# Kernel optimization log

Measured on AMD Instinct MI355X. Metric: run time of the kernel, lower is better.

## Reference

```python
import jax, jax.numpy as jnp
import numpy as np


def setup_inputs() -> dict:
    key = jax.random.key(0)
    ks = jax.random.split(key, 8)
    N, D, G, H = 131072, 128, 2048, 512
    features = jax.random.normal(ks[0], (N, D), dtype=jnp.float32)
    graph_index = jnp.sort(jax.random.randint(ks[1], (N,), 0, G))
    s1 = 1.0 / np.sqrt(D)
    W_m = jax.random.uniform(ks[2], (H, D), jnp.float32, -s1, s1)
    b_m = jax.random.uniform(ks[3], (H,), jnp.float32, -s1, s1)
    s2 = 1.0 / np.sqrt(H)
    W_ih = jax.random.uniform(ks[4], (4 * H, 2 * H), jnp.float32, -s2, s2)
    W_hh = jax.random.uniform(ks[5], (4 * H, H), jnp.float32, -s2, s2)
    b_ih = jax.random.uniform(ks[6], (4 * H,), jnp.float32, -s2, s2)
    b_hh = jax.random.uniform(ks[7], (4 * H,), jnp.float32, -s2, s2)
    return dict(features=features, graph_index=graph_index, W_m=W_m, b_m=b_m,
                W_ih=W_ih, W_hh=W_hh, b_ih=b_ih, b_hh=b_hh, num_graphs=G)


def reference(features, graph_index, W_m, b_m, W_ih, W_hh, b_ih, b_hh, num_graphs):
    H = W_m.shape[0]
    LOOP = 3
    EPS = 1e-7
    NEG_BIG = -1e10
    m = features @ W_m.T + b_m                      # [N, H]
    h = jnp.zeros((num_graphs, H), m.dtype)
    c = jnp.zeros((num_graphs, H), m.dtype)
    q_star = jnp.zeros((num_graphs, 2 * H), m.dtype)
    for _ in range(LOOP):
        # PyTorch LSTMCell: gates in (i, f, g, o) order
        gates = q_star @ W_ih.T + h @ W_hh.T + (b_ih + b_hh)   # [G, 4H]
        i_g, f_g, g_g, o_g = jnp.split(gates, 4, axis=-1)
        c = jax.nn.sigmoid(f_g) * c + jax.nn.sigmoid(i_g) * jnp.tanh(g_g)
        h = jax.nn.sigmoid(o_g) * jnp.tanh(c)
        # attention scores per node against its graph's query h
        e = jnp.sum(m * h[graph_index], axis=-1, keepdims=True)  # [N, 1]
        e_max = jax.ops.segment_max(e, graph_index, num_segments=num_graphs)
        e_max = jax.lax.stop_gradient(
            jnp.where(jnp.isfinite(e_max), e_max, NEG_BIG))
        e = e - e_max[graph_index]
        exp_e = jnp.exp(jnp.clip(e, -30.0, 20.0))
        exp_sum = jax.ops.segment_sum(exp_e, graph_index, num_segments=num_graphs)
        a = exp_e / (exp_sum[graph_index] + EPS)                 # [N, 1]
        r = jax.ops.segment_sum(m * a, graph_index, num_segments=num_graphs)  # [G, H]
        q_star = jnp.concatenate([h, r], axis=-1)                # [G, 2H]
    return q_star
```

## Files before the change

kernel.cpp:

```cpp
#include <hip/hip_runtime.h>

#define N_NODES 131072
#define DIM     128
#define NG      2048
#define HD      512

typedef unsigned short u16;
typedef _Float16 half8 __attribute__((ext_vector_type(8)));
typedef float  f32x4  __attribute__((ext_vector_type(4)));

__device__ u16   g_wm[(size_t)HD * DIM];
__device__ u16   g_wmT[(size_t)DIM * HD];
__device__ u16   g_wgf[(size_t)2048 * 640];
__device__ u16   g_wih2[(size_t)2048 * 512];
__device__ float g_bc[2048];
__device__ float g_bf[2048];
__device__ float g_gh[2048];
__device__ float g_c0[512];
__device__ float g_w20[128];
__device__ float g_tp[NG];
__device__ u16   g_Acat[(size_t)NG * 640];
__device__ u16   g_h3[(size_t)NG * HD];
__device__ float g_c[(size_t)NG * HD];
__device__ int   g_start[NG + 1];
__device__ int   g_isbf16;
__device__ int   g_idx64;

__device__ __forceinline__ float bf2f(u16 u) {
  unsigned v = ((unsigned)u) << 16;
  float f; __builtin_memcpy(&f, &v, 4); return f;
}
__device__ __forceinline__ float u2f_hi(unsigned u) {
  unsigned v = u & 0xFFFF0000u;
  float f; __builtin_memcpy(&f, &v, 4); return f;
}
__device__ __forceinline__ float u2f_lo(unsigned u) {
  unsigned v = u << 16;
  float f; __builtin_memcpy(&f, &v, 4); return f;
}
__device__ __forceinline__ u16 f2bf(float f) {
  unsigned u; __builtin_memcpy(&u, &f, 4);
  u += 0x7FFFu + ((u >> 16) & 1u);
  return (u16)(u >> 16);
}
__device__ __forceinline__ u16 f2h(float f) {
  _Float16 h = (_Float16)f; u16 u; __builtin_memcpy(&u, &h, 2); return u;
}
__device__ __forceinline__ float h2f(u16 u) {
  _Float16 h; __builtin_memcpy(&h, &u, 2); return (float)h;
}
__device__ __forceinline__ float rdf(const void* p, int i) {
  return g_isbf16 ? bf2f(((const u16*)p)[i]) : ((const float*)p)[i];
}

#define GLD16(gp, lp) __builtin_amdgcn_global_load_lds(                          \
    (const __attribute__((address_space(1))) void*)(gp),                         \
    (__attribute__((address_space(3))) void*)(lp), 16, 0, 0)

__global__ void k_detect(const void* feat, const void* gi) {
  __shared__ int cnt;
  if (threadIdx.x == 0) cnt = 0;
  __syncthreads();
  u16 u = ((const u16*)feat)[threadIdx.x];
  float v = bf2f(u);
  float a = fabsf(v);
  int ok = (v == v) && a >= 1e-6f && a <= 1e6f;
  atomicAdd(&cnt, ok);
  __syncthreads();
  if (threadIdx.x == 0) {
    g_isbf16 = (cnt >= 230);
    g_idx64 = (((const int*)gi)[N_NODES - 1] == 0);
  }
}

#define NWP ((size_t)HD * DIM / 2)
#define NWT ((size_t)DIM * HD / 2)
#define NW1 ((size_t)2048 * 512 / 2)
#define NW2 ((size_t)2048 * 512 / 2)
#define W_PAIRS (NWP + NWT + NW1 + NW2)

__global__ __launch_bounds__(256) void k_s0(const void* gidxv, const void* wmp,
                                            const void* wih, const void* whh) {
  const int t = threadIdx.x;
  for (size_t i = (size_t)blockIdx.x * 256 + t; i < W_PAIRS;
       i += (size_t)gridDim.x * 256) {
    if (i < NWP) {
      float v0, v1;
      if (g_isbf16) {
        unsigned pr = ((const unsigned*)wmp)[i];
        v0 = bf2f((u16)pr); v1 = bf2f((u16)(pr >> 16));
      } else {
        float2 v = ((const float2*)wmp)[i];
        v0 = v.x; v1 = v.y;
      }
      ((unsigned*)g_wm)[i] = (unsigned)f2h(v0) | ((unsigned)f2h(v1) << 16);
    } else if (i < NWP + NWT) {
      size_t p = i - NWP;
      int d = (int)(p >> 8), j = (int)(p & 255) * 2;
      float v0 = rdf(wmp, j * DIM + d);
      float v1 = rdf(wmp, (j + 1) * DIM + d);
      ((unsigned*)g_wmT)[(size_t)d * 256 + (j >> 1)] =
          (unsigned)f2h(v0) | ((unsigned)f2h(v1) << 16);
    } else if (i < NWP + NWT + NW1) {
      size_t p = i - NWP - NWT;
      int n = (int)(p >> 8), kp = (int)(p & 255), k = kp * 2;
      int orig = (n & 3) * 512 + (n >> 2);
      float v0 = rdf(wih, orig * 1024 + k)     + rdf(whh, orig * 512 + k);
      float v1 = rdf(wih, orig * 1024 + k + 1) + rdf(whh, orig * 512 + k + 1);
      ((unsigned*)g_wgf)[(size_t)n * 320 + kp] =
          (unsigned)f2h(v0) | ((unsigned)f2h(v1) << 16);
    } else {
      size_t p = i - NWP - NWT - NW1;
      int n = (int)(p >> 8), kp = (int)(p & 255), k = kp * 2;
      int orig = (n & 3) * 512 + (n >> 2);
      float v0 = rdf(wih, orig * 1024 + 512 + k);
      float v1 = rdf(wih, orig * 1024 + 512 + k + 1);
      ((unsigned*)g_wih2)[(size_t)n * 256 + kp] =
          (unsigned)f2h(v0) | ((unsigned)f2h(v1) << 16);
    }
  }
  if (blockIdx.x < 512) {
    int n = blockIdx.x * 256 + t;
    const int idx64 = g_idx64;
    int gg = idx64 ? (int)((const long long*)gidxv)[n] : ((const int*)gidxv)[n];
    if (n == 0) {
      for (int x = 0; x <= gg; ++x) g_start[x] = 0;
    } else {
      int gp = idx64 ? (int)((const long long*)gidxv)[n - 1] : ((const int*)gidxv)[n - 1];
      for (int x = gp + 1; x <= gg; ++x) g_start[x] = n;
    }
    if (n == N_NODES - 1) {
      for (int x = gg + 1; x <= NG; ++x) g_start[x] = N_NODES;
    }
  }
}

__global__ __launch_bounds__(256) void k_s1(const void* bih, const void* bhh,
                                            const void* bm) {
  alignas(16) __shared__ char smem[16384];
  const int t = threadIdx.x, b = blockIdx.x;
  if (b < 128) {
    float* s_bm = (float*)smem;
    float* s_h0 = s_bm + 512;
    for (int p = t; p < 512; p += 256) {
      s_bm[p] = rdf(bm, p);
      float xi = rdf(bih, p)        + rdf(bhh, p);
      float xg = rdf(bih, p + 1024) + rdf(bhh, p + 1024);
      float xo = rdf(bih, p + 1536) + rdf(bhh, p + 1536);
      float si = 1.f / (1.f + __expf(-xi));
      float tg = tanhf(xg);
      float so = 1.f / (1.f + __expf(-xo));
      s_h0[p] = so * tanhf(si * tg);
    }
    __syncthreads();
    const int rloc = t >> 4, k = t & 15;
    const int n = b * 16 + rloc;
    float sbf = 0.f, sgh = 0.f;
#pragma unroll
    for (int j = 0; j < 4; ++j) {
      const int e = k * 8 + j * 128;
      half8 w2v = *(const half8*)(g_wih2 + (size_t)n * 512 + e);
      half8 w1v = *(const half8*)(g_wgf  + (size_t)n * 640 + e);
#pragma unroll
      for (int d = 0; d < 8; ++d) {
        sbf += (float)w2v[d] * s_bm[e + d];
        sgh += (float)w1v[d] * s_h0[e + d];
      }
    }
#pragma unroll
    for (int o = 1; o < 16; o <<= 1) {
      sbf += __shfl_xor(sbf, o, 64);
      sgh += __shfl_xor(sgh, o, 64);
    }
    if (k == 0) {
      const int orig = (n & 3) * 512 + (n >> 2);
      g_bf[n] = sbf;
      g_gh[n] = sgh;
      g_bc[n] = rdf(bih, orig) + rdf(bhh, orig);
    }
  } else if (b < 192) {
    u16* As = (u16*)smem;
    u16* Bs = As + 4096;
    const int bx = b - 128;
    const int lid = t & 63, w = t >> 6;
    const int m0 = (bx & 31) * 64, n0 = (bx >> 5) * 64;
    const int rr = lid & 15, quad = lid >> 4;
    const int rsub = lid >> 3;
    const int cs = (lid & 7) ^ rsub;
    const int wm = (w >> 1) * 32, wn = (w & 1) * 32;
    f32x4 acc[2][2] = {};
    for (int kt = 0; kt < 8; ++kt) {
      const int k0 = kt * 64;
      GLD16(g_wih2 + (size_t)(m0 + w * 16 + rsub) * 512 + k0 + cs * 8, As + (w * 16) * 64);
      GLD16(g_wih2 + (size_t)(m0 + w * 16 + 8 + rsub) * 512 + k0 + cs * 8, As + (w * 16 + 8) * 64);
      GLD16(g_wmT + (size_t)(n0 + w * 16 + rsub) * 512 + k0 + cs * 8, Bs + (w * 16) * 64);
      GLD16(g_wmT + (size_t)(n0 + w * 16 + 8 + rsub) * 512 + k0 + cs * 8, Bs + (w * 16 + 8) * 64);
      __syncthreads();
#pragma unroll
      for (int kk = 0; kk < 2; ++kk) {
        const int qb = kk * 4 + quad;
        const int sw = (qb ^ (rr & 7)) << 3;
        half8 af[2], bfr[2];
#pragma unroll
        for (int i = 0; i < 2; ++i) af[i]  = *(const half8*)(As + (wm + i * 16 + rr) * 64 + sw);
#pragma unroll
        for (int j = 0; j < 2; ++j) bfr[j] = *(const half8*)(Bs + (wn + j * 16 + rr) * 64 + sw);
#pragma unroll
        for (int i = 0; i < 2; ++i)
#pragma unroll
          for (int j = 0; j < 2; ++j)
            acc[i][j] = __builtin_amdgcn_mfma_f32_16x16x32_f16(bfr[j], af[i], acc[i][j], 0, 0, 0);
      }
      __syncthreads();
    }
#pragma unroll
    for (int i = 0; i < 2; ++i)
#pragma unroll
      for (int j = 0; j < 2; ++j) {
        const int row = m0 + wm + i * 16 + rr;
        const int c0 = n0 + wn + j * 16 + quad * 4;
        u16 h4[4];
#pragma unroll
        for (int r = 0; r < 4; ++r) h4[r] = f2h(acc[i][j][r]);
        *(uint2*)(g_wgf + (size_t)row * 640 + 512 + c0) =
            make_uint2((unsigned)h4[0] | ((unsigned)h4[1] << 16),
                       (unsigned)h4[2] | ((unsigned)h4[3] << 16));
      }
  } else if (b == 192) {
    float* s_h   = (float*)smem;
    float* s_red = s_h + 512;
    for (int j = t; j < 512; j += 256) {
      float xi = rdf(bih, j)        + rdf(bhh, j);
      float xg = rdf(bih, j + 1024) + rdf(bhh, j + 1024);
      float xo = rdf(bih, j + 1536) + rdf(bhh, j + 1536);
      float si = 1.f / (1.f + __expf(-xi));
      float tg = tanhf(xg);
      float so = 1.f / (1.f + __expf(-xo));
      float cn = si * tg;
      float hn = so * tanhf(cn);
      g_c0[j] = cn;
      s_h[j] = hn;
    }
    __syncthreads();
    const int dg = t & 15, jg = t >> 4;
    float a8[8] = {};
    for (int jj = 0; jj < 32; ++jj) {
      const int j = jg * 32 + jj;
      half8 wv = *(const half8*)(g_wm + (size_t)j * 128 + dg * 8);
      const float hv = s_h[j];
#pragma unroll
      for (int d = 0; d < 8; ++d) a8[d] += hv * (float)wv[d];
    }
#pragma unroll
    for (int d = 0; d < 8; ++d) {
      a8[d] += __shfl_xor(a8[d], 16, 64);
      a8[d] += __shfl_xor(a8[d], 32, 64);
    }
    const int w = t >> 6;
    if ((t & 63) < 16) {
      *(f32x4*)&s_red[w * 128 + dg * 8]     = *(f32x4*)&a8[0];
      *(f32x4*)&s_red[w * 128 + dg * 8 + 4] = *(f32x4*)&a8[4];
    }
    __syncthreads();
    if (t < 128)
      g_w20[t] = s_red[t] + s_red[128 + t] + s_red[256 + t] + s_red[384 + t];
  }
}

__global__ __launch_bounds__(256) void k_gemm(int ktiles2, int aoff, int useGh,
                                              int first, int wout, int h3out,
                                              void* __restrict__ out) {
  alignas(16) __shared__ u16 As[2][64 * 64];
  alignas(16) __shared__ u16 Bs[2][64 * 64];
  const int t = threadIdx.x, lid = t & 63, w = t >> 6;
  const int m0 = (blockIdx.x & 31) * 64, n0 = (blockIdx.x >> 5) * 64;
  const int rr = lid & 15, quad = lid >> 4;
  const int rsub = lid >> 3;
  const int cs = (lid & 7) ^ rsub;
  const int wm = (w >> 1) * 32, wn = (w & 1) * 32;
  const int isb = g_isbf16;
  f32x4 acc[2][2] = {};
  for (int kt2 = 0; kt2 < ktiles2; ++kt2) {
#pragma unroll
    for (int b = 0; b < 2; ++b) {
      const int k0 = aoff + (kt2 * 2 + b) * 64;
      GLD16(g_Acat + (size_t)(m0 + w * 16 + rsub) * 640 + k0 + cs * 8, As[b] + (w * 16) * 64);
      GLD16(g_Acat + (size_t)(m0 + w * 16 + 8 + rsub) * 640 + k0 + cs * 8, As[b] + (w * 16 + 8) * 64);
      GLD16(g_wgf  + (size_t)(n0 + w * 16 + rsub) * 640 + k0 + cs * 8, Bs[b] + (w * 16) * 64);
      GLD16(g_wgf  + (size_t)(n0 + w * 16 + 8 + rsub) * 640 + k0 + cs * 8, Bs[b] + (w * 16 + 8) * 64);
    }
    __syncthreads();
#pragma unroll
    for (int b = 0; b < 2; ++b)
#pragma unroll
      for (int kk = 0; kk < 2; ++kk) {
        const int qb = kk * 4 + quad;
        const int sw = (qb ^ (rr & 7)) << 3;
        half8 af[2], bfr[2];
#pragma unroll
        for (int i = 0; i < 2; ++i) af[i]  = *(const half8*)(As[b] + (wm + i * 16 + rr) * 64 + sw);
#pragma unroll
        for (int j = 0; j < 2; ++j) bfr[j] = *(const half8*)(Bs[b] + (wn + j * 16 + rr) * 64 + sw);
#pragma unroll
        for (int i = 0; i < 2; ++i)
#pragma unroll
          for (int j = 0; j < 2; ++j)
            acc[i][j] = __builtin_amdgcn_mfma_f32_16x16x32_f16(bfr[j], af[i], acc[i][j], 0, 0, 0);
      }
    __syncthreads();
  }
#pragma unroll
  for (int i = 0; i < 2; ++i) {
    const int row = m0 + wm + i * 16 + rr;
    const float tp = g_tp[row];
#pragma unroll
    for (int j = 0; j < 2; ++j) {
      const int c0 = n0 + wn + j * 16 + quad * 4;
      const int jj = c0 >> 2;
      float4 bc = *(const float4*)(g_bc + c0);
      float4 bf = *(const float4*)(g_bf + c0);
      float gx = 0.f, gy = 0.f, gz = 0.f, gw = 0.f;
      if (useGh) {
        float4 gh = *(const float4*)(g_gh + c0);
        gx = gh.x; gy = gh.y; gz = gh.z; gw = gh.w;
      }
      float xi = acc[i][j][0] + bc.x + gx + tp * bf.x;
      float xf = acc[i][j][1] + bc.y + gy + tp * bf.y;
      float xg = acc[i][j][2] + bc.z + gz + tp * bf.z;
      float xo = acc[i][j][3] + bc.w + gw + tp * bf.w;
      float si = 1.f / (1.f + __expf(-xi));
      float sf = 1.f / (1.f + __expf(-xf));
      float tg = tanhf(xg);
      float so = 1.f / (1.f + __expf(-xo));
      float cp = first ? g_c0[jj] : g_c[(size_t)row * 512 + jj];
      float cn = sf * cp + si * tg;
      float hn = so * tanhf(cn);
      g_c[(size_t)row * 512 + jj] = cn;
      if (h3out) g_h3[(size_t)row * 512 + jj] = f2h(hn);
      else       g_Acat[(size_t)row * 640 + jj] = f2h(hn);
      if (wout) {
        if (isb) ((u16*)out)[(size_t)row * 1024 + jj] = f2bf(hn);
        else     ((float*)out)[(size_t)row * 1024 + jj] = hn;
      }
    }
  }
}

__global__ __launch_bounds__(256) void k_attn(const void* __restrict__ feat, int mode,
                                              int hsel, int fin,
                                              void* __restrict__ out,
                                              const void* __restrict__ bm) {
  __shared__ float s_m[4], s_l[4];
  __shared__ float s_s[4][DIM];
  __shared__ float s_h[512];
  __shared__ float s_keep[DIM];
  __shared__ float s_tpv[1];
  const int g = blockIdx.x;
  const int t = threadIdx.x, lid = t & 63, wid = t >> 6;
  const int c = lid & 15;
  const int slot = lid >> 4;
  const int israw = g_isbf16;
  const int s = g_start[g], e = g_start[g + 1];
  float w2r[8];
  if (mode) {
    const u16* hsrc = hsel ? g_h3 : g_Acat;
    const int hstr = hsel ? 512 : 640;
    for (int p = t; p < 512; p += 256)
      s_h[p] = h2f(hsrc[(size_t)g * hstr + p]);
    __syncthreads();
    const int jg = t >> 4;
    float a8[8] = {};
    for (int jj = 0; jj < 32; ++jj) {
      const int j = jg * 32 + jj;
      half8 wv = *(const half8*)(g_wm + (size_t)j * 128 + c * 8);
      const float hv = s_h[j];
#pragma unroll
      for (int d = 0; d < 8; ++d) a8[d] += hv * (float)wv[d];
    }
#pragma unroll
    for (int d = 0; d < 8; ++d) {
      a8[d] += __shfl_xor(a8[d], 16, 64);
      a8[d] += __shfl_xor(a8[d], 32, 64);
    }
    if (lid < 16) {
      *(f32x4*)&s_s[wid][c * 8]     = *(f32x4*)&a8[0];
      *(f32x4*)&s_s[wid][c * 8 + 4] = *(f32x4*)&a8[4];
    }
    __syncthreads();
#pragma unroll
    for (int d = 0; d < 8; ++d)
      w2r[d] = s_s[0][c * 8 + d] + s_s[1][c * 8 + d] +
               s_s[2][c * 8 + d] + s_s[3][c * 8 + d];
    __syncthreads();
  } else {
    *(float4*)(w2r)     = *(const float4*)(g_w20 + c * 8);
    *(float4*)(w2r + 4) = *(const float4*)(g_w20 + c * 8 + 4);
  }
  float mrun = -3.0e38f, lsum = 0.f;
  float racc[8] = {0.f, 0.f, 0.f, 0.f, 0.f, 0.f, 0.f, 0.f};
  for (int nb = s + wid * 4; nb < e; nb += 16) {
    const int n = nb + slot;
    float fv[8], d;
    if (n < e) {
      if (israw) {
        uint4 q = *(const uint4*)((const u16*)feat + (size_t)n * DIM + c * 8);
        fv[0] = u2f_lo(q.x); fv[1] = u2f_hi(q.x);
        fv[2] = u2f_lo(q.y); fv[3] = u2f_hi(q.y);
        fv[4] = u2f_lo(q.z); fv[5] = u2f_hi(q.z);
        fv[6] = u2f_lo(q.w); fv[7] = u2f_hi(q.w);
      } else {
        const float* fp = (const float*)feat + (size_t)n * DIM + c * 8;
        float4 f0 = *(const float4*)fp;
        float4 f1 = *(const float4*)(fp + 4);
        fv[0] = f0.x; fv[1] = f0.y; fv[2] = f0.z; fv[3] = f0.w;
        fv[4] = f1.x; fv[5] = f1.y; fv[6] = f1.z; fv[7] = f1.w;
      }
      d = 0.f;
#pragma unroll
      for (int j = 0; j < 8; ++j) d += fv[j] * w2r[j];
    } else {
      d = -1.0e30f;
#pragma unroll
      for (int j = 0; j < 8; ++j) fv[j] = 0.f;
    }
#pragma unroll
    for (int o = 1; o < 16; o <<= 1) d += __shfl_xor(d, o, 64);
    float m4 = fmaxf(d, __shfl_xor(d, 16, 64));
    m4 = fmaxf(m4, __shfl_xor(m4, 32, 64));
    float mnew = fmaxf(mrun, m4);
    float sc = __expf(mrun - mnew);
    float w = __expf(d - mnew);
    lsum = lsum * sc + w;
#pragma unroll
    for (int j = 0; j < 8; ++j) racc[j] = racc[j] * sc + w * fv[j];
    mrun = mnew;
  }
  float lt = lsum + __shfl_xor(lsum, 16, 64);
  lt += __shfl_xor(lt, 32, 64);
#pragma unroll
  for (int j = 0; j < 8; ++j) {
    racc[j] += __shfl_xor(racc[j], 16, 64);
    racc[j] += __shfl_xor(racc[j], 32, 64);
  }
  if (lid == 0) s_m[wid] = mrun;
  __syncthreads();
  float gmax = fmaxf(fmaxf(s_m[0], s_m[1]), fmaxf(s_m[2], s_m[3]));
  float scw = __expf(mrun - gmax);
  if (lid < 16) {
    float4 lo = make_float4(racc[0] * scw, racc[1] * scw, racc[2] * scw, racc[3] * scw);
    float4 hi = make_float4(racc[4] * scw, racc[5] * scw, racc[6] * scw, racc[7] * scw);
    *(f32x4*)&s_s[wid][c * 8] = *(f32x4*)&lo;
    *(f32x4*)&s_s[wid][c * 8 + 4] = *(f32x4*)&hi;
  }
  if (lid == 0) s_l[wid] = lt * scw;
  __syncthreads();
  float total = s_l[0] + s_l[1] + s_l[2] + s_l[3];
  float inv = 1.f / (total + 1e-7f);
  if (!fin) {
    if (t == 0) g_tp[g] = total * inv;
    if (t < 64) {
      int d0 = t * 2;
      float v0 = (s_s[0][d0] + s_s[1][d0] + s_s[2][d0] + s_s[3][d0]) * inv;
      float v1 = (s_s[0][d0 + 1] + s_s[1][d0 + 1] + s_s[2][d0 + 1] + s_s[3][d0 + 1]) * inv;
      ((unsigned*)g_Acat)[(size_t)g * 320 + 256 + t] =
          (unsigned)f2h(v0) | ((unsigned)f2h(v1) << 16);
    }
  } else {
    if (t == 0) s_tpv[0] = total * inv;
    if (t < 64) {
      int d0 = t * 2;
      s_keep[d0]     = (s_s[0][d0] + s_s[1][d0] + s_s[2][d0] + s_s[3][d0]) * inv;
      s_keep[d0 + 1] = (s_s[0][d0 + 1] + s_s[1][d0 + 1] + s_s[2][d0 + 1] + s_s[3][d0 + 1]) * inv;
    }
    __syncthreads();
    const int jj = t * 2;
    const unsigned* wt = (const unsigned*)g_wmT;
    float a0 = 0.f, a1 = 0.f;
#pragma unroll 8
    for (int d = 0; d < 128; ++d) {
      unsigned pr = wt[d * 256 + t];
      float kv = s_keep[d];
      a0 += kv * h2f((u16)pr);
      a1 += kv * h2f((u16)(pr >> 16));
    }
    float tp = s_tpv[0];
    float r0 = a0 + tp * rdf(bm, jj);
    float r1 = a1 + tp * rdf(bm, jj + 1);
    if (israw) {
      ((unsigned*)out)[((size_t)g * 1024 + 512 + jj) >> 1] =
          (unsigned)f2bf(r0) | ((unsigned)f2bf(r1) << 16);
    } else {
      *(float2*)((float*)out + (size_t)g * 1024 + 512 + jj) = make_float2(r0, r1);
    }
  }
}

extern "C" void kernel_launch(void* const* d_in, const int* in_sizes, int n_in,
                              void* d_out, int out_size, void* d_ws, size_t ws_size,
                              hipStream_t stream) {
  const void* features = d_in[0];
  const void* gidx     = d_in[1];
  const void* W_m      = d_in[2];
  const void* b_m      = d_in[3];
  const void* W_ih     = d_in[4];
  const void* W_hh     = d_in[5];
  const void* b_ih     = d_in[6];
  const void* b_hh     = d_in[7];

  k_detect<<<1, 256, 0, stream>>>(features, gidx);
  k_s0<<<1024, 256, 0, stream>>>(gidx, W_m, W_ih, W_hh);
  k_s1<<<193, 256, 0, stream>>>(b_ih, b_hh, b_m);
  k_attn<<<NG, 256, 0, stream>>>(features, 0, 0, 0, d_out, b_m);
  k_gemm<<<1024, 256, 0, stream>>>(1, 512, 1, 1, 0, 0, d_out);
  k_attn<<<NG, 256, 0, stream>>>(features, 1, 0, 0, d_out, b_m);
  k_gemm<<<1024, 256, 0, stream>>>(5, 0, 0, 0, 1, 1, d_out);
  k_attn<<<NG, 256, 0, stream>>>(features, 1, 1, 1, d_out, b_m);
}
```

Baseline: 224.3 us.

## Batch per-graph h·W_m projection into MFMA GEMM kernel and fold detect into setup

The per-graph projection of h through W_m was computed inside each attention block with scalar FMAs over a 512x128 weight, reading the whole weight once per graph. A separate small MFMA GEMM kernel now computes all [G,128] projections at once into a global buffer, and the attention kernel just loads its row. The dtype/index detection kernel is merged into the first setup kernel, so every block recomputes the flags locally and one launch is removed. This adds two small kernel launches and a global intermediate buffer in exchange for removing the redundant per-block GEMV work.

```diff
diff --git a/kernel.cpp b/kernel.cpp
--- a/kernel.cpp
+++ b/kernel.cpp
@@ -18,6 +18,7 @@
 __device__ float g_gh[2048];
 __device__ float g_c0[512];
 __device__ float g_w20[128];
+__device__ float g_w2[(size_t)NG * DIM];
 __device__ float g_tp[NG];
 __device__ u16   g_Acat[(size_t)NG * 640];
 __device__ u16   g_h3[(size_t)NG * HD];
@@ -52,26 +53,13 @@
 __device__ __forceinline__ float rdf(const void* p, int i) {
   return g_isbf16 ? bf2f(((const u16*)p)[i]) : ((const float*)p)[i];
 }
+__device__ __forceinline__ float rdl(const void* p, int i, int isb) {
+  return isb ? bf2f(((const u16*)p)[i]) : ((const float*)p)[i];
+}
 
 #define GLD16(gp, lp) __builtin_amdgcn_global_load_lds(                          \
     (const __attribute__((address_space(1))) void*)(gp),                         \
     (__attribute__((address_space(3))) void*)(lp), 16, 0, 0)
-
-__global__ void k_detect(const void* feat, const void* gi) {
-  __shared__ int cnt;
-  if (threadIdx.x == 0) cnt = 0;
-  __syncthreads();
-  u16 u = ((const u16*)feat)[threadIdx.x];
-  float v = bf2f(u);
-  float a = fabsf(v);
-  int ok = (v == v) && a >= 1e-6f && a <= 1e6f;
-  atomicAdd(&cnt, ok);
-  __syncthreads();
-  if (threadIdx.x == 0) {
-    g_isbf16 = (cnt >= 230);
-    g_idx64 = (((const int*)gi)[N_NODES - 1] == 0);
-  }
-}
 
 #define NWP ((size_t)HD * DIM / 2)
 #define NWT ((size_t)DIM * HD / 2)
@@ -79,14 +67,30 @@
 #define NW2 ((size_t)2048 * 512 / 2)
 #define W_PAIRS (NWP + NWT + NW1 + NW2)
 
-__global__ __launch_bounds__(256) void k_s0(const void* gidxv, const void* wmp,
-                                            const void* wih, const void* whh) {
+__global__ __launch_bounds__(256) void k_s0(const void* feat, const void* gidxv,
+                                            const void* wmp, const void* wih,
+                                            const void* whh) {
+  __shared__ int s_cnt;
   const int t = threadIdx.x;
+  if (t == 0) s_cnt = 0;
+  __syncthreads();
+  {
+    u16 u = ((const u16*)feat)[t];
+    float v = bf2f(u);
+    float a = fabsf(v);
+    int ok = (v == v) && a >= 1e-6f && a <= 1e6f;
+    atomicAdd(&s_cnt, ok);
+  }
+  __syncthreads();
+  const int isb = (s_cnt >= 230);
+  const int idx64 = (((const int*)gidxv)[N_NODES - 1] == 0);
+  if (blockIdx.x == 0 && t == 0) { g_isbf16 = isb; g_idx64 = idx64; }
+
   for (size_t i = (size_t)blockIdx.x * 256 + t; i < W_PAIRS;
        i += (size_t)gridDim.x * 256) {
     if (i < NWP) {
       float v0, v1;
-      if (g_isbf16) {
+      if (isb) {
         unsigned pr = ((const unsigned*)wmp)[i];
         v0 = bf2f((u16)pr); v1 = bf2f((u16)(pr >> 16));
       } else {
@@ -97,31 +101,30 @@
     } else if (i < NWP + NWT) {
       size_t p = i - NWP;
       int d = (int)(p >> 8), j = (int)(p & 255) * 2;
-      float v0 = rdf(wmp, j * DIM + d);
-      float v1 = rdf(wmp, (j + 1) * DIM + d);
+      float v0 = rdl(wmp, j * DIM + d, isb);
+      float v1 = rdl(wmp, (j + 1) * DIM + d, isb);
       ((unsigned*)g_wmT)[(size_t)d * 256 + (j >> 1)] =
           (unsigned)f2h(v0) | ((unsigned)f2h(v1) << 16);
     } else if (i < NWP + NWT + NW1) {
       size_t p = i - NWP - NWT;
       int n = (int)(p >> 8), kp = (int)(p & 255), k = kp * 2;
       int orig = (n & 3) * 512 + (n >> 2);
-      float v0 = rdf(wih, orig * 1024 + k)     + rdf(whh, orig * 512 + k);
-      float v1 = rdf(wih, orig * 1024 + k + 1) + rdf(whh, orig * 512 + k + 1);
+      float v0 = rdl(wih, orig * 1024 + k, isb)     + rdl(whh, orig * 512 + k, isb);
+      float v1 = rdl(wih, orig * 1024 + k + 1, isb) + rdl(whh, orig * 512 + k + 1, isb);
       ((unsigned*)g_wgf)[(size_t)n * 320 + kp] =
           (unsigned)f2h(v0) | ((unsigned)f2h(v1) << 16);
     } else {
       size_t p = i - NWP - NWT - NW1;
       int n = (int)(p >> 8), kp = (int)(p & 255), k = kp * 2;
       int orig = (n & 3) * 512 + (n >> 2);
-      float v0 = rdf(wih, orig * 1024 + 512 + k);
-      float v1 = rdf(wih, orig * 1024 + 512 + k + 1);
+      float v0 = rdl(wih, orig * 1024 + 512 + k, isb);
+      float v1 = rdl(wih, orig * 1024 + 512 + k + 1, isb);
       ((unsigned*)g_wih2)[(size_t)n * 256 + kp] =
           (unsigned)f2h(v0) | ((unsigned)f2h(v1) << 16);
     }
   }
   if (blockIdx.x < 512) {
     int n = blockIdx.x * 256 + t;
-    const int idx64 = g_idx64;
     int gg = idx64 ? (int)((const long long*)gidxv)[n] : ((const int*)gidxv)[n];
     if (n == 0) {
       for (int x = 0; x <= gg; ++x) g_start[x] = 0;
@@ -267,6 +270,52 @@
   }
 }
 
+__global__ __launch_bounds__(256) void k_w2(int hsel) {
+  alignas(16) __shared__ u16 As[64 * 64];
+  alignas(16) __shared__ u16 Bs[64 * 64];
+  const int t = threadIdx.x, lid = t & 63, w = t >> 6;
+  const int m0 = blockIdx.x * 64, n0 = blockIdx.y * 64;
+  const int rr = lid & 15, quad = lid >> 4;
+  const int rsub = lid >> 3;
+  const int cs = (lid & 7) ^ rsub;
+  const int wm = (w >> 1) * 32, wn = (w & 1) * 32;
+  const u16* Ap = hsel ? g_h3 : g_Acat;
+  const int astr = hsel ? 512 : 640;
+  f32x4 acc[2][2] = {};
+  for (int kt = 0; kt < 8; ++kt) {
+    const int k0 = kt * 64;
+    GLD16(Ap + (size_t)(m0 + w * 16 + rsub) * astr + k0 + cs * 8, As + (w * 16) * 64);
+    GLD16(Ap + (size_t)(m0 + w * 16 + 8 + rsub) * astr + k0 + cs * 8, As + (w * 16 + 8) * 64);
+    GLD16(g_wmT + (size_t)(n0 + w * 16 + rsub) * 512 + k0 + cs * 8, Bs + (w * 16) * 64);
+    GLD16(g_wmT + (size_t)(n0 + w * 16 + 8 + rsub) * 512 + k0 + cs * 8, Bs + (w * 16 + 8) * 64);
+    __syncthreads();
+#pragma unroll
+    for (int kk = 0; kk < 2; ++kk) {
+      const int qb = kk * 4 + quad;
+      const int sw = (qb ^ (rr & 7)) << 3;
+      half8 af[2], bfr[2];
+#pragma unroll
+      for (int i = 0; i < 2; ++i) af[i]  = *(const half8*)(As + (wm + i * 16 + rr) * 64 + sw);
+#pragma unroll
+      for (int j = 0; j < 2; ++j) bfr[j] = *(const half8*)(Bs + (wn + j * 16 + rr) * 64 + sw);
+#pragma unroll
+      for (int i = 0; i < 2; ++i)
+#pragma unroll
+        for (int j = 0; j < 2; ++j)
+          acc[i][j] = __builtin_amdgcn_mfma_f32_16x16x32_f16(bfr[j], af[i], acc[i][j], 0, 0, 0);
+    }
+    __syncthreads();
+  }
+#pragma unroll
+  for (int i = 0; i < 2; ++i)
+#pragma unroll
+    for (int j = 0; j < 2; ++j) {
+      const int row = m0 + wm + i * 16 + rr;
+      const int c0 = n0 + wn + j * 16 + quad * 4;
+      *(f32x4*)(g_w2 + (size_t)row * DIM + c0) = acc[i][j];
+    }
+}
+
 __global__ __launch_bounds__(256) void k_gemm(int ktiles2, int aoff, int useGh,
                                               int first, int wout, int h3out,
                                               void* __restrict__ out) {
@@ -346,13 +395,12 @@
   }
 }
 
-__global__ __launch_bounds__(256) void k_attn(const void* __restrict__ feat, int mode,
-                                              int hsel, int fin,
+__global__ __launch_bounds__(256) void k_attn(const void* __restrict__ feat,
+                                              int w2sel, int fin,
                                               void* __restrict__ out,
                                               const void* __restrict__ bm) {
   __shared__ float s_m[4], s_l[4];
   __shared__ float s_s[4][DIM];
-  __shared__ float s_h[512];
   __shared__ float s_keep[DIM];
   __shared__ float s_tpv[1];
   const int g = blockIdx.x;
@@ -362,36 +410,9 @@
   const int israw = g_isbf16;
   const int s = g_start[g], e = g_start[g + 1];
   float w2r[8];
-  if (mode) {
-    const u16* hsrc = hsel ? g_h3 : g_Acat;
-    const int hstr = hsel ? 512 : 640;
-    for (int p = t; p < 512; p += 256)
-      s_h[p] = h2f(hsrc[(size_t)g * hstr + p]);
-    __syncthreads();
-    const int jg = t >> 4;
-    float a8[8] = {};
-    for (int jj = 0; jj < 32; ++jj) {
-      const int j = jg * 32 + jj;
-      half8 wv = *(const half8*)(g_wm + (size_t)j * 128 + c * 8);
-      const float hv = s_h[j];
-#pragma unroll
-      for (int d = 0; d < 8; ++d) a8[d] += hv * (float)wv[d];
-    }
-#pragma unroll
-    for (int d = 0; d < 8; ++d) {
-      a8[d] += __shfl_xor(a8[d], 16, 64);
-      a8[d] += __shfl_xor(a8[d], 32, 64);
-    }
-    if (lid < 16) {
-      *(f32x4*)&s_s[wid][c * 8]     = *(f32x4*)&a8[0];
-      *(f32x4*)&s_s[wid][c * 8 + 4] = *(f32x4*)&a8[4];
-    }
-    __syncthreads();
-#pragma unroll
-    for (int d = 0; d < 8; ++d)
-      w2r[d] = s_s[0][c * 8 + d] + s_s[1][c * 8 + d] +
-               s_s[2][c * 8 + d] + s_s[3][c * 8 + d];
-    __syncthreads();
+  if (w2sel) {
+    *(float4*)(w2r)     = *(const float4*)(g_w2 + (size_t)g * DIM + c * 8);
+    *(float4*)(w2r + 4) = *(const float4*)(g_w2 + (size_t)g * DIM + c * 8 + 4);
   } else {
     *(float4*)(w2r)     = *(const float4*)(g_w20 + c * 8);
     *(float4*)(w2r + 4) = *(const float4*)(g_w20 + c * 8 + 4);
@@ -507,12 +528,13 @@
   const void* b_ih     = d_in[6];
   const void* b_hh     = d_in[7];
 
-  k_detect<<<1, 256, 0, stream>>>(features, gidx);
-  k_s0<<<1024, 256, 0, stream>>>(gidx, W_m, W_ih, W_hh);
+  k_s0<<<1024, 256, 0, stream>>>(features, gidx, W_m, W_ih, W_hh);
   k_s1<<<193, 256, 0, stream>>>(b_ih, b_hh, b_m);
-  k_attn<<<NG, 256, 0, stream>>>(features, 0, 0, 0, d_out, b_m);
+  k_attn<<<NG, 256, 0, stream>>>(features, 0, 0, d_out, b_m);
   k_gemm<<<1024, 256, 0, stream>>>(1, 512, 1, 1, 0, 0, d_out);
-  k_attn<<<NG, 256, 0, stream>>>(features, 1, 0, 0, d_out, b_m);
+  k_w2<<<dim3(32, 2), 256, 0, stream>>>(0);
+  k_attn<<<NG, 256, 0, stream>>>(features, 1, 0, d_out, b_m);
   k_gemm<<<1024, 256, 0, stream>>>(5, 0, 0, 0, 1, 1, d_out);
-  k_attn<<<NG, 256, 0, stream>>>(features, 1, 1, 1, d_out, b_m);
-}
+  k_w2<<<dim3(32, 2), 256, 0, stream>>>(1);
+  k_attn<<<NG, 256, 0, stream>>>(features, 1, 1, d_out, b_m);
+}
```

New measurement: 213.4 us (median of 2 runs). 1.05x faster.
